# Kernel tuning notes

Measured on AMD Instinct MI355X. Metric: run time of the kernel, lower is better.

The kernel has to match this reference:

```python
import jax, jax.numpy as jnp
import numpy as np

NQ = 4
PI_HALF = np.pi / 2
HAD = jnp.array([[1, 1], [1, -1]], dtype=jnp.complex64) / np.sqrt(2)
CNOT = jnp.array([[1, 0, 0, 0], [0, 1, 0, 0], [0, 0, 0, 1], [0, 0, 1, 0]], dtype=jnp.complex64)
_bits = (np.arange(2 ** NQ)[:, None] >> np.arange(NQ - 1, -1, -1)[None, :]) & 1
ZSIGNS = jnp.asarray(1.0 - 2.0 * _bits, jnp.float32)  # [16, NQ]


def _ry(theta):
    c = jnp.cos(theta / 2).astype(jnp.complex64)
    s = jnp.sin(theta / 2).astype(jnp.complex64)
    return jnp.stack([jnp.stack([c, -s], -1), jnp.stack([s, c], -1)], -2)  # [...,2,2]


def _rot(phi, theta, omega):
    # PennyLane Rot = RZ(omega) @ RY(theta) @ RZ(phi)
    c = jnp.cos(theta / 2).astype(jnp.complex64)
    s = jnp.sin(theta / 2).astype(jnp.complex64)
    ep = jnp.exp(0.5j * phi).astype(jnp.complex64)
    eo = jnp.exp(0.5j * omega).astype(jnp.complex64)
    return jnp.stack([jnp.stack([jnp.conj(ep) * jnp.conj(eo) * c, -ep * jnp.conj(eo) * s]),
                      jnp.stack([jnp.conj(ep) * eo * s, ep * eo * c])])


def _cry(theta):
    # controlled-RY, batched: [B] -> [B,4,4], basis order (control, target)
    B = theta.shape[0]
    U = jnp.zeros((B, 4, 4), jnp.complex64).at[:, 0, 0].set(1.0).at[:, 1, 1].set(1.0)
    return U.at[:, 2:, 2:].set(_ry(theta))


def _apply1(state, U, wire):
    s = jnp.moveaxis(state, wire + 1, 1)
    shp = s.shape
    s = s.reshape(shp[0], 2, -1)
    s = jnp.einsum('ij,bjk->bik', U, s) if U.ndim == 2 else jnp.einsum('bij,bjk->bik', U, s)
    return jnp.moveaxis(s.reshape(shp), 1, wire + 1)


def _apply2(state, U, q0, q1):
    s = jnp.moveaxis(state, (q0 + 1, q1 + 1), (1, 2))
    shp = s.shape
    s = s.reshape(shp[0], 4, -1)
    s = jnp.einsum('ij,bjk->bik', U, s) if U.ndim == 2 else jnp.einsum('bij,bjk->bik', U, s)
    return jnp.moveaxis(s.reshape(shp), (1, 2), (q0 + 1, q1 + 1))


def _init_state(B):
    s = jnp.zeros((B, 2 ** NQ), jnp.complex64).at[:, 0].set(1.0)
    return s.reshape((B,) + (2,) * NQ)


def _zexp(state):
    p = state.reshape(state.shape[0], -1)
    p = p.real ** 2 + p.imag ** 2
    return p @ ZSIGNS  # [B, NQ]


def _attention_circuit(q, k, params):
    # q, k: [E, NQ] angles; params: [NQ, 3] shared
    s = _init_state(q.shape[0])
    for i in range(NQ):
        s = _apply1(s, _ry(q[:, i]), i)
    for i in range(NQ):
        s = _apply1(s, HAD, i)
    for i in range(NQ):
        s = _apply2(s, _cry(k[:, i]), i, (i + 1) % NQ)
    for i in range(NQ):
        s = _apply1(s, _rot(params[i, 0], params[i, 1], params[i, 2]), i)
    return _zexp(s)


def _entangle_circuit(x, params):
    # x: [N, NQ] angles; params: [n_layers, NQ, 3]
    s = _init_state(x.shape[0])
    for i in range(NQ):
        s = _apply1(s, _ry(x[:, i]), i)
    for l in range(params.shape[0]):
        for i in range(NQ - 1):
            s = _apply2(s, CNOT, i, i + 1)
        for i in range(NQ):
            s = _apply1(s, _rot(params[l, i, 0], params[l, i, 1], params[l, i, 2]), i)
        s = _apply2(s, CNOT, 0, NQ - 1)  # n_qubits >= 4
    return _zexp(s)


def _path_circuit(x, params):
    # x: [N, NQ]; params: [3, NQ, 3]
    s = _init_state(x.shape[0])
    for i in range(NQ):
        s = _apply1(s, HAD, i)
    for i in range(NQ):
        s = _apply1(s, _ry(x[:, i]), i)
    for l in range(3):
        for i in range(NQ):
            s = _apply1(s, _rot(params[l, i, 0], params[l, i, 1], params[l, i, 2]), i)
        for i in range(NQ - 1):
            s = _apply2(s, CNOT, i, i + 1)
    return _zexp(s)


def _forward(x, W_in, b_in, lin_W, lin_b, qproj_W, qproj_b, ent_params,
             attq_W, attq_b, attk_W, attk_b, att_qp, path_params,
             path_in_W, path_in_b, path_out_W, path_out_b, out_W, out_b, edge_index):
    N = x.shape[0]
    loops = jnp.arange(N, dtype=edge_index.dtype)
    ei = jnp.concatenate([edge_index, jnp.stack([loops, loops])], axis=1)  # add_self_loops
    src, dst = ei[0], ei[1]
    h = jax.nn.relu(x @ W_in.T + b_in)
    for l in range(lin_W.shape[0]):
        x_cls = h @ lin_W[l].T + lin_b[l]
        xq = _entangle_circuit(jnp.tanh(h[:, :NQ]) * PI_HALF, ent_params[l])
        x_comb = x_cls + xq @ qproj_W[l].T + qproj_b[l]
        q = jnp.tanh(h @ attq_W[l].T + attq_b[l]) * PI_HALF
        k = jnp.tanh(h @ attk_W[l].T + attk_b[l]) * PI_HALF
        scores = _attention_circuit(q[src], k[dst], att_qp[l]).mean(axis=1)  # [E]
        att = jax.nn.softmax(scores)  # global softmax over all edges (faithful)
        h = jax.ops.segment_sum(att[:, None] * x_comb[src], dst, num_segments=N)
        h = jax.nn.relu(h)  # dropout is identity at eval
    pq = jnp.tanh(h @ path_in_W.T + path_in_b) * PI_HALF
    h = _path_circuit(pq, path_params) @ path_out_W.T + path_out_b
    return h @ out_W.T + out_b


def setup_inputs() -> dict:
    key = jax.random.key(0)
    ks = jax.random.split(key, 22)
    N, E, D_in, D_h, D_out, L = 20000, 300000, 64, 128, 32, 2
    w = lambda k, shape: jax.random.normal(k, shape, jnp.float32) * 0.1
    return {
        'x': jax.random.normal(ks[0], (N, D_in), jnp.float32),
        'W_in': w(ks[1], (D_h, D_in)), 'b_in': w(ks[2], (D_h,)),
        'lin_W': w(ks[3], (L, D_h, D_h)), 'lin_b': w(ks[4], (L, D_h)),
        'qproj_W': w(ks[5], (L, D_h, NQ)), 'qproj_b': w(ks[6], (L, D_h)),
        'ent_params': w(ks[7], (L, 2, NQ, 3)),
        'attq_W': w(ks[8], (L, NQ, D_h)), 'attq_b': w(ks[9], (L, NQ)),
        'attk_W': w(ks[10], (L, NQ, D_h)), 'attk_b': w(ks[11], (L, NQ)),
        'att_qp': w(ks[12], (L, NQ, 3)),
        'path_params': w(ks[13], (3, NQ, 3)),
        'path_in_W': w(ks[14], (NQ, D_h)), 'path_in_b': w(ks[15], (NQ,)),
        'path_out_W': w(ks[16], (D_h, NQ)), 'path_out_b': w(ks[17], (D_h,)),
        'out_W': w(ks[18], (D_out, D_h)), 'out_b': w(ks[19], (D_out,)),
        'edge_index': jax.random.randint(ks[20], (2, E), 0, N, dtype=jnp.int32),
    }


def reference(x, W_in, b_in, lin_W, lin_b, qproj_W, qproj_b, ent_params,
              attq_W, attq_b, attk_W, attk_b, att_qp, path_params,
              path_in_W, path_in_b, path_out_W, path_out_b, out_W, out_b, edge_index):
    return _forward(x, W_in, b_in, lin_W, lin_b, qproj_W, qproj_b, ent_params,
                    attq_W, attq_b, attk_W, attk_b, att_qp, path_params,
                    path_in_W, path_in_b, path_out_W, path_out_b, out_W, out_b, edge_index)
```

## Files before the change

### kernel.cpp

```cpp
#include <hip/hip_runtime.h>
#include <math.h>

#define PI_HALF 1.57079632679489662f

__device__ __forceinline__ float fast_tanh(float x) {
    float e = __expf(2.f * x);
    return 1.f - 2.f * __builtin_amdgcn_rcpf(e + 1.f);
}


__device__ __forceinline__ void prod_init(float sr[16],
        float c0, float s0, float c1, float s1,
        float c2, float s2, float c3, float s3) {
    float p2[4];
    p2[0] = c0 * c1; p2[1] = c0 * s1; p2[2] = s0 * c1; p2[3] = s0 * s1;
    float p3[8];
#pragma unroll
    for (int j = 0; j < 4; ++j) { p3[2 * j] = p2[j] * c2; p3[2 * j + 1] = p2[j] * s2; }
#pragma unroll
    for (int j = 0; j < 8; ++j) { sr[2 * j] = p3[j] * c3; sr[2 * j + 1] = p3[j] * s3; }
}

template<int M>
__device__ __forceinline__ void had_r(float sr[16]) {
    const float r = 0.70710678118654752f;
#pragma unroll
    for (int i = 0; i < 16; ++i) {
        if (i & M) continue;
        const int j = i | M;
        float ar = sr[i], br = sr[j];
        sr[i] = (ar + br) * r;
        sr[j] = (ar - br) * r;
    }
}

template<int MC, int MT>
__device__ __forceinline__ void cry_r(float sr[16], float c, float s) {
#pragma unroll
    for (int i = 0; i < 16; ++i) {
        if (!(i & MC) || (i & MT)) continue;
        const int j = i | MT;
        float ar = sr[i], br = sr[j];
        sr[i] = c * ar - s * br;
        sr[j] = s * ar + c * br;
    }
}

template<int MC, int MT>
__device__ __forceinline__ void cnot_r(float sr[16]) {
#pragma unroll
    for (int i = 0; i < 16; ++i) {
        if (!(i & MC) || (i & MT)) continue;
        const int j = i | MT;
        float t = sr[i]; sr[i] = sr[j]; sr[j] = t;
    }
}

template<int MC, int MT>
__device__ __forceinline__ void cnot_g(float sr[16], float si[16]) {
#pragma unroll
    for (int i = 0; i < 16; ++i) {
        if (!(i & MC) || (i & MT)) continue;
        const int j = i | MT;
        float tr = sr[i], ti = si[i];
        sr[i] = sr[j]; si[i] = si[j];
        sr[j] = tr;    si[j] = ti;
    }
}

template<int M>
__device__ __forceinline__ void rot_pre(float sr[16], float si[16], const float* __restrict__ u) {
    const float u00r = u[0], u00i = u[1], u01r = u[2], u01i = u[3];
    const float u10r = u[4], u10i = u[5], u11r = u[6], u11i = u[7];
#pragma unroll
    for (int i = 0; i < 16; ++i) {
        if (i & M) continue;
        const int j = i | M;
        float ar = sr[i], ai = si[i], br = sr[j], bi = si[j];
        sr[i] = u00r * ar - u00i * ai + u01r * br - u01i * bi;
        si[i] = u00r * ai + u00i * ar + u01r * bi + u01i * br;
        sr[j] = u10r * ar - u10i * ai + u11r * br - u11i * bi;
        si[j] = u10r * ai + u10i * ar + u11r * bi + u11i * br;
    }
}

template<int M>
__device__ __forceinline__ void rot_first(float sr[16], float si[16], const float* __restrict__ u) {
    const float u00r = u[0], u00i = u[1], u01r = u[2], u01i = u[3];
    const float u10r = u[4], u10i = u[5], u11r = u[6], u11i = u[7];
#pragma unroll
    for (int i = 0; i < 16; ++i) {
        if (i & M) continue;
        const int j = i | M;
        float ar = sr[i], br = sr[j];
        sr[i] = u00r * ar + u01r * br;
        si[i] = u00i * ar + u01i * br;
        sr[j] = u10r * ar + u11r * br;
        si[j] = u10i * ar + u11i * br;
    }
}

__device__ __forceinline__ void zexp_g(const float sr[16], const float si[16], float z[4]) {
    float p[16];
#pragma unroll
    for (int i = 0; i < 16; ++i) p[i] = sr[i] * sr[i] + si[i] * si[i];
    z[0] = z[1] = z[2] = z[3] = 0.f;
#pragma unroll
    for (int i = 0; i < 16; ++i) {
        z[0] += (i & 8) ? -p[i] : p[i];
        z[1] += (i & 4) ? -p[i] : p[i];
        z[2] += (i & 2) ? -p[i] : p[i];
        z[3] += (i & 1) ? -p[i] : p[i];
    }
}


__global__ void k_fsi(const int* __restrict__ ei, int* __restrict__ cur,
                      int* __restrict__ srcs, int* __restrict__ inv, int E, int EP,
                      const float* __restrict__ entp, const float* __restrict__ attqp,
                      const float* __restrict__ pparm,
                      const float* __restrict__ outW, const float* __restrict__ outb,
                      const float* __restrict__ poW, const float* __restrict__ pob,
                      float* __restrict__ rotbuf, float* __restrict__ M,
                      float* __restrict__ v,
                      const float* __restrict__ x, const float* __restrict__ W,
                      const float* __restrict__ b, float* __restrict__ h,
                      int N, int eblocks) {
    __shared__ float xs[32 * 64];
    const int bb = blockIdx.x;
    const int tid = threadIdx.x;
    if (bb < eblocks) {
        int e = bb * 256 + tid;
        if (e < EP) {
            int s_, d_;
            if (e < E) { s_ = ei[e]; d_ = ei[E + e]; } else { s_ = d_ = e - E; }
            int pos = atomicAdd(&cur[d_], 1);
            srcs[pos] = s_;
            inv[e] = pos;
        }
        return;
    }
    if (bb == eblocks) {
        const int t = tid;
        if (t < 36) {
            const float* p;
            if (t < 16)      p = entp  + t * 3;
            else if (t < 24) p = attqp + (t - 16) * 3;
            else             p = pparm + (t - 24) * 3;
            float phi = p[0], theta = p[1], omega = p[2];
            float st, ct; sincosf(0.5f * theta, &st, &ct);
            float sp, cp; sincosf(0.5f * (phi + omega), &sp, &cp);
            float sm, cm; sincosf(0.5f * (phi - omega), &sm, &cm);
            float* u = rotbuf + t * 8;
            u[0] =  ct * cp;  u[1] = -ct * sp;
            u[2] = -st * cm;  u[3] = -st * sm;
            u[4] =  st * cm;  u[5] = -st * sm;
            u[6] =  ct * cp;  u[7] =  ct * sp;
        } else if (t >= 64 && t < 192) {
            int t2 = t - 64;
            int o = t2 >> 2, i = t2 & 3;
            float acc = 0.f;
            for (int j = 0; j < 128; ++j) acc += outW[o * 128 + j] * poW[j * 4 + i];
            M[t2] = acc;
        } else if (t >= 192 && t < 224) {
            int o = t - 192;
            float acc = outb[o];
            for (int j = 0; j < 128; ++j) acc += outW[o * 128 + j] * pob[j];
            v[o] = acc;
        }
        return;
    }
    const int base = (bb - eblocks - 1) * 32;
    for (int idx = tid; idx < 32 * 64; idx += 256) {
        int n = base + (idx >> 6);
        xs[idx] = (n < N) ? x[(size_t)n * 64 + (idx & 63)] : 0.f;
    }
    __syncthreads();
    const int ch = tid & 127;
    const int half = tid >> 7;
    float acc[16];
#pragma unroll
    for (int n = 0; n < 16; ++n) acc[n] = 0.f;
    const float4* wr4 = (const float4*)(W + ch * 64);
    for (int c4 = 0; c4 < 16; ++c4) {
        float4 w = wr4[c4];
#pragma unroll
        for (int n = 0; n < 16; ++n) {
            float4 hv = *(const float4*)&xs[(half * 16 + n) * 64 + c4 * 4];
            acc[n] += w.x * hv.x + w.y * hv.y + w.z * hv.z + w.w * hv.w;
        }
    }
    const float bbv = b[ch];
#pragma unroll
    for (int n = 0; n < 16; ++n) {
        int node = base + half * 16 + n;
        if (node < N) h[(size_t)node * 128 + ch] = fmaxf(acc[n] + bbv, 0.f);
    }
}

#define HS_STRIDE 132
__global__ void k_entlin(const float* __restrict__ h, const float* __restrict__ rotE2,
                         const float* __restrict__ linW, const float* __restrict__ linb,
                         const float* __restrict__ qpW, const float* __restrict__ qpb,
                         const float* __restrict__ aqW, const float* __restrict__ aqb,
                         const float* __restrict__ akW, const float* __restrict__ akb,
                         float* __restrict__ xcomb, float* __restrict__ qbuf,
                         float* __restrict__ kbuf, int N) {
    __shared__ float hs[16 * HS_STRIDE];
    __shared__ float xqs[16 * 4];
    const int base = blockIdx.x * 16;
    const int tid = threadIdx.x;
    for (int idx = tid; idx < 16 * 32; idx += 128) {
        int n = idx >> 5, c4 = idx & 31;
        int node = base + n;
        float4 hv = (node < N) ? *(const float4*)&h[(size_t)node * 128 + c4 * 4]
                               : make_float4(0.f, 0.f, 0.f, 0.f);
        *(float4*)&hs[n * HS_STRIDE + c4 * 4] = hv;
    }
    __syncthreads();
    if (tid < 64) {
#pragma unroll
        for (int rep = 0; rep < 2; ++rep) {
            const int dt = tid + rep * 64;
            const int nl = dt >> 3;
            const int which = dt & 7;
            const int qi = which & 3;
            const float4* Wp4 = (const float4*)(((which < 4) ? aqW : akW) + qi * 128);
            float dot = (which < 4) ? aqb[qi] : akb[qi];
            for (int c4 = 0; c4 < 32; ++c4) {
                float4 w = Wp4[c4];
                float4 hv = *(const float4*)&hs[nl * HS_STRIDE + c4 * 4];
                dot += w.x * hv.x + w.y * hv.y + w.z * hv.z + w.w * hv.w;
            }
            int node = base + nl;
            if (node < N) {
                float halfang = fast_tanh(dot) * (0.5f * PI_HALF);
                float s, c; __sincosf(halfang, &s, &c);
                float* dst = ((which < 4) ? qbuf : kbuf) + (size_t)node * 8 + qi * 2;
                dst[0] = c; dst[1] = s;
            }
        }
    } else if (tid < 80) {
        const int nl = tid - 64;
        if (base + nl < N) {
            float4 hv = *(const float4*)&hs[nl * HS_STRIDE];
            float c0, s0, c1, s1, c2, s2, c3, s3;
            { float a = fast_tanh(hv.x) * (0.5f * PI_HALF); __sincosf(a, &s0, &c0); }
            { float a = fast_tanh(hv.y) * (0.5f * PI_HALF); __sincosf(a, &s1, &c1); }
            { float a = fast_tanh(hv.z) * (0.5f * PI_HALF); __sincosf(a, &s2, &c2); }
            { float a = fast_tanh(hv.w) * (0.5f * PI_HALF); __sincosf(a, &s3, &c3); }
            float sr[16], si[16];
            prod_init(sr, c0, s0, c1, s1, c2, s2, c3, s3);
            cnot_r<8, 4>(sr); cnot_r<4, 2>(sr); cnot_r<2, 1>(sr);
            rot_first<8>(sr, si, rotE2);
            rot_pre<4>(sr, si, rotE2 + 8);
            rot_pre<2>(sr, si, rotE2 + 16);
            rot_pre<1>(sr, si, rotE2 + 24);
            cnot_g<8, 1>(sr, si);
            cnot_g<8, 4>(sr, si); cnot_g<4, 2>(sr, si); cnot_g<2, 1>(sr, si);
            const float* P = rotE2 + 32;
            rot_pre<8>(sr, si, P);
            rot_pre<4>(sr, si, P + 8);
            rot_pre<2>(sr, si, P + 16);
            rot_pre<1>(sr, si, P + 24);
            cnot_g<8, 1>(sr, si);
            float z[4]; zexp_g(sr, si, z);
            xqs[nl * 4 + 0] = z[0]; xqs[nl * 4 + 1] = z[1];
            xqs[nl * 4 + 2] = z[2]; xqs[nl * 4 + 3] = z[3];
        }
    }
    __syncthreads();
    const int lane = tid & 63;
    const int nh = tid >> 6;
    const int ch0 = lane, ch1 = lane + 64;
    float acc0[8], acc1[8];
#pragma unroll
    for (int n = 0; n < 8; ++n) { acc0[n] = 0.f; acc1[n] = 0.f; }
    const float4* w04 = (const float4*)(linW + ch0 * 128);
    const float4* w14 = (const float4*)(linW + ch1 * 128);
    for (int c4 = 0; c4 < 32; ++c4) {
        float4 wa = w04[c4];
        float4 wb = w14[c4];
#pragma unroll
        for (int n = 0; n < 8; ++n) {
            float4 hv = *(const float4*)&hs[(nh * 8 + n) * HS_STRIDE + c4 * 4];
            acc0[n] += wa.x * hv.x + wa.y * hv.y + wa.z * hv.z + wa.w * hv.w;
            acc1[n] += wb.x * hv.x + wb.y * hv.y + wb.z * hv.z + wb.w * hv.w;
        }
    }
    const float b0 = linb[ch0] + qpb[ch0];
    const float b1 = linb[ch1] + qpb[ch1];
    const float q00 = qpW[ch0 * 4 + 0], q01 = qpW[ch0 * 4 + 1];
    const float q02 = qpW[ch0 * 4 + 2], q03 = qpW[ch0 * 4 + 3];
    const float q10 = qpW[ch1 * 4 + 0], q11 = qpW[ch1 * 4 + 1];
    const float q12 = qpW[ch1 * 4 + 2], q13 = qpW[ch1 * 4 + 3];
#pragma unroll
    for (int n = 0; n < 8; ++n) {
        const int nl = nh * 8 + n;
        const int node = base + nl;
        if (node < N) {
            float x0 = xqs[nl * 4 + 0], x1 = xqs[nl * 4 + 1];
            float x2 = xqs[nl * 4 + 2], x3 = xqs[nl * 4 + 3];
            xcomb[(size_t)node * 128 + ch0] = acc0[n] + b0
                + q00 * x0 + q01 * x1 + q02 * x2 + q03 * x3;
            xcomb[(size_t)node * 128 + ch1] = acc1[n] + b1
                + q10 * x0 + q11 * x1 + q12 * x2 + q13 * x3;
        }
    }
}

__global__ void k_att(const float* __restrict__ qb, const float* __restrict__ kb,
                      const int* __restrict__ ei, const float* __restrict__ RA,
                      const int* __restrict__ inv, float* __restrict__ escore,
                      float* __restrict__ sumexp, int E, int EP) {
    __shared__ float red[4];
    int e = blockIdx.x * blockDim.x + threadIdx.x;
    float ex = 0.f;
    if (e < EP) {
        int s_, d_;
        if (e < E) { s_ = ei[e]; d_ = ei[E + e]; } else { s_ = d_ = e - E; }
        float4 qa = *(const float4*)&qb[(size_t)s_ * 8];
        float4 qc = *(const float4*)&qb[(size_t)s_ * 8 + 4];
        float4 ka = *(const float4*)&kb[(size_t)d_ * 8];
        float4 kc = *(const float4*)&kb[(size_t)d_ * 8 + 4];
        float sr[16], si[16];
        prod_init(sr, qa.x, qa.y, qa.z, qa.w, qc.x, qc.y, qc.z, qc.w);
        had_r<8>(sr); had_r<4>(sr); had_r<2>(sr); had_r<1>(sr);
        cry_r<8, 4>(sr, ka.x, ka.y);
        cry_r<4, 2>(sr, ka.z, ka.w);
        cry_r<2, 1>(sr, kc.x, kc.y);
        cry_r<1, 8>(sr, kc.z, kc.w);
        rot_first<8>(sr, si, RA);
        rot_pre<4>(sr, si, RA + 8);
        rot_pre<2>(sr, si, RA + 16);
        rot_pre<1>(sr, si, RA + 24);
        float p0  = sr[0]  * sr[0]  + si[0]  * si[0];
        float p1  = sr[1]  * sr[1]  + si[1]  * si[1];
        float p2  = sr[2]  * sr[2]  + si[2]  * si[2];
        float p4  = sr[4]  * sr[4]  + si[4]  * si[4];
        float p8  = sr[8]  * sr[8]  + si[8]  * si[8];
        float p7  = sr[7]  * sr[7]  + si[7]  * si[7];
        float p11 = sr[11] * sr[11] + si[11] * si[11];
        float p13 = sr[13] * sr[13] + si[13] * si[13];
        float p14 = sr[14] * sr[14] + si[14] * si[14];
        float p15 = sr[15] * sr[15] + si[15] * si[15];
        float sc = (p0 - p15) + 0.5f * ((p1 + p2 + p4 + p8) - (p7 + p11 + p13 + p14));
        ex = __expf(sc);
        escore[inv[e]] = ex;
    }
    float wsum = ex;
#pragma unroll
    for (int d = 32; d; d >>= 1) wsum += __shfl_xor(wsum, d, 64);
    if ((threadIdx.x & 63) == 0) red[threadIdx.x >> 6] = wsum;
    __syncthreads();
    if (threadIdx.x == 0) atomicAdd(sumexp, red[0] + red[1] + red[2] + red[3]);
}


__global__ void k_hist(const int* __restrict__ ei, int* __restrict__ cnt, int E, int EP) {
    int e = blockIdx.x * blockDim.x + threadIdx.x;
    if (e >= EP) return;
    int d_ = (e < E) ? ei[E + e] : e - E;
    atomicAdd(&cnt[d_], 1);
}

__global__ void k_scan(const int* __restrict__ cnt, int* __restrict__ off,
                       int* __restrict__ cur, int N) {
    __shared__ int tot[1024];
    const int t = threadIdx.x;
    const int chunk = (N + 1023) >> 10;
    const int s0 = t * chunk;
    const int s1 = min(s0 + chunk, N);
    int sum = 0;
    for (int i = s0; i < s1; ++i) sum += cnt[i];
    tot[t] = sum;
    __syncthreads();
    for (int d = 1; d < 1024; d <<= 1) {
        int v = (t >= d) ? tot[t - d] : 0;
        __syncthreads();
        tot[t] += v;
        __syncthreads();
    }
    int run = (t == 0) ? 0 : tot[t - 1];
    for (int i = s0; i < s1; ++i) {
        off[i] = run; cur[i] = run;
        run += cnt[i];
    }
}

__global__ void k_gather(const float* __restrict__ xcomb, const int* __restrict__ srcs,
                         const float* __restrict__ escore, const int* __restrict__ off,
                         const int* __restrict__ cnt, const float* __restrict__ sumexp,
                         float* __restrict__ h) {
    __shared__ int sS[128];
    __shared__ float wS[128];
    const int b = blockIdx.x;
    const int tid = threadIdx.x;
    const int start = off[b];
    const int num = cnt[b];
    float acc = 0.f;
    for (int base = 0; base < num; base += 128) {
        int m = min(128, num - base);
        if (tid < m) {
            sS[tid] = srcs[start + base + tid];
            wS[tid] = escore[start + base + tid];
        }
        __syncthreads();
        for (int i = 0; i < m; ++i)
            acc += wS[i] * xcomb[(size_t)sS[i] * 128 + tid];
        __syncthreads();
    }
    const float invS = __builtin_amdgcn_rcpf(sumexp[0]);
    h[(size_t)b * 128 + tid] = fmaxf(acc * invS, 0.f);
}

__global__ void k_tail(const float* __restrict__ h, const float* __restrict__ piW,
                       const float* __restrict__ pib, const float* __restrict__ RP,
                       const float* __restrict__ M, const float* __restrict__ v,
                       float* __restrict__ out, int N) {
    __shared__ float pqS[64 * 8];
    __shared__ float zS[64 * 4];
    __shared__ float MS[128];
    __shared__ float vS[32];
    const int tid = threadIdx.x;
    const int base = blockIdx.x * 64;
    if (tid < 128) MS[tid] = M[tid];
    else if (tid < 160) vS[tid - 128] = v[tid - 128];
    {
        const int nl = tid >> 2, i = tid & 3;
        const int node = base + nl;
        if (node < N) {
            float dot = pib[i];
            const float4* w4 = (const float4*)(piW + i * 128);
            const float4* h4 = (const float4*)(h + (size_t)node * 128);
#pragma unroll 8
            for (int c4 = 0; c4 < 32; ++c4) {
                float4 w = w4[c4];
                float4 hv = h4[c4];
                dot += w.x * hv.x + w.y * hv.y + w.z * hv.z + w.w * hv.w;
            }
            float halfang = fast_tanh(dot) * (0.5f * PI_HALF);
            float s, c; __sincosf(halfang, &s, &c);
            pqS[nl * 8 + i * 2]     = c;
            pqS[nl * 8 + i * 2 + 1] = s;
        }
    }
    __syncthreads();
    if (tid < 64 && base + tid < N) {
        const float r = 0.70710678118654752f;
        float c0 = pqS[tid * 8 + 0], s0 = pqS[tid * 8 + 1];
        float c1 = pqS[tid * 8 + 2], s1 = pqS[tid * 8 + 3];
        float c2 = pqS[tid * 8 + 4], s2 = pqS[tid * 8 + 5];
        float c3 = pqS[tid * 8 + 6], s3 = pqS[tid * 8 + 7];
        float u0 = r * (c0 - s0), w0 = r * (c0 + s0);
        float u1 = r * (c1 - s1), w1 = r * (c1 + s1);
        float u2 = r * (c2 - s2), w2 = r * (c2 + s2);
        float u3 = r * (c3 - s3), w3 = r * (c3 + s3);
        float sr[16], si[16];
        prod_init(sr, u0, w0, u1, w1, u2, w2, u3, w3);
        rot_first<8>(sr, si, RP);
        rot_pre<4>(sr, si, RP + 8);
        rot_pre<2>(sr, si, RP + 16);
        rot_pre<1>(sr, si, RP + 24);
        cnot_g<8, 4>(sr, si); cnot_g<4, 2>(sr, si); cnot_g<2, 1>(sr, si);
#pragma unroll
        for (int l = 1; l < 3; ++l) {
            const float* P = RP + l * 32;
            rot_pre<8>(sr, si, P);
            rot_pre<4>(sr, si, P + 8);
            rot_pre<2>(sr, si, P + 16);
            rot_pre<1>(sr, si, P + 24);
            cnot_g<8, 4>(sr, si); cnot_g<4, 2>(sr, si); cnot_g<2, 1>(sr, si);
        }
        float z[4]; zexp_g(sr, si, z);
        zS[tid * 4 + 0] = z[0]; zS[tid * 4 + 1] = z[1];
        zS[tid * 4 + 2] = z[2]; zS[tid * 4 + 3] = z[3];
    }
    __syncthreads();
#pragma unroll
    for (int k = 0; k < 8; ++k) {
        int flat = k * 256 + tid;
        int nl = flat >> 5;
        int o = flat & 31;
        int node = base + nl;
        if (node < N) {
            out[(size_t)node * 32 + o] = vS[o]
                + MS[o * 4 + 0] * zS[nl * 4 + 0] + MS[o * 4 + 1] * zS[nl * 4 + 1]
                + MS[o * 4 + 2] * zS[nl * 4 + 2] + MS[o * 4 + 3] * zS[nl * 4 + 3];
        }
    }
}


extern "C" void kernel_launch(void* const* d_in, const int* in_sizes, int n_in,
                              void* d_out, int out_size, void* d_ws, size_t ws_size,
                              hipStream_t stream) {
    const float* x     = (const float*)d_in[0];
    const float* W_in  = (const float*)d_in[1];
    const float* b_in  = (const float*)d_in[2];
    const float* linW  = (const float*)d_in[3];
    const float* linb  = (const float*)d_in[4];
    const float* qpW   = (const float*)d_in[5];
    const float* qpb   = (const float*)d_in[6];
    const float* entp  = (const float*)d_in[7];
    const float* aqW   = (const float*)d_in[8];
    const float* aqb   = (const float*)d_in[9];
    const float* akW   = (const float*)d_in[10];
    const float* akb   = (const float*)d_in[11];
    const float* attqp = (const float*)d_in[12];
    const float* pparm = (const float*)d_in[13];
    const float* piW   = (const float*)d_in[14];
    const float* pib   = (const float*)d_in[15];
    const float* poW   = (const float*)d_in[16];
    const float* pob   = (const float*)d_in[17];
    const float* outW  = (const float*)d_in[18];
    const float* outb  = (const float*)d_in[19];
    const int*   ei    = (const int*)d_in[20];

    const int N  = in_sizes[0] / 64;
    const int E  = in_sizes[20] / 2;
    const int EP = E + N;

    float* ws     = (float*)d_ws;
    float* h      = ws;
    float* xcomb  = h      + (size_t)N * 128;
    float* qbuf   = xcomb  + (size_t)N * 128;
    float* kbuf   = qbuf   + (size_t)N * 8;
    float* escore = kbuf   + (size_t)N * 8;
    float* rotbuf = escore + EP;
    float* Mm     = rotbuf + 36 * 8;
    float* vv     = Mm + 128;
    int*   cnt    = (int*)(vv + 32);
    float* sumexp = (float*)(cnt + N);
    int*   off    = (int*)(sumexp + 4);
    int*   cur    = off + N;
    int*   srcs   = cur + N;
    int*   inv    = srcs + EP;

    const float* rotE = rotbuf;
    const float* rotA = rotbuf + 128;
    const float* rotP = rotbuf + 192;

    const int nb16 = (N + 15) / 16;
    const int nb32 = (N + 31) / 32;
    const int ebl  = (EP + 255) / 256;

    hipMemsetAsync(cnt, 0, (size_t)(N + 4) * sizeof(int), stream);
    k_hist<<<ebl, 256, 0, stream>>>(ei, cnt, E, EP);
    k_scan<<<1, 1024, 0, stream>>>(cnt, off, cur, N);
    k_fsi<<<ebl + 1 + nb32, 256, 0, stream>>>(ei, cur, srcs, inv, E, EP,
                                              entp, attqp, pparm, outW, outb, poW, pob,
                                              rotbuf, Mm, vv, x, W_in, b_in, h, N, ebl);

    for (int l = 0; l < 2; ++l) {
        k_entlin<<<nb16, 128, 0, stream>>>(h, rotE + l * 64,
            linW + (size_t)l * 128 * 128, linb + l * 128,
            qpW + (size_t)l * 128 * 4, qpb + l * 128,
            aqW + (size_t)l * 4 * 128, aqb + l * 4,
            akW + (size_t)l * 4 * 128, akb + l * 4,
            xcomb, qbuf, kbuf, N);
        k_att<<<ebl, 256, 0, stream>>>(qbuf, kbuf, ei, rotA + l * 32, inv,
                                       escore, sumexp + l, E, EP);
        k_gather<<<N, 128, 0, stream>>>(xcomb, srcs, escore, off, cnt, sumexp + l, h);
    }

    k_tail<<<(N + 63) / 64, 256, 0, stream>>>(h, piW, pib, rotP, Mm, vv, (float*)d_out, N);
}
```

Before: 355.5 us.

## Fuse attention scoring into gather and defer softmax normalization to consumers

Per-edge attention score computation moves into the per-destination gather kernel, so the escore/inv buffers and the separate k_att launch disappear. Because the global sum is no longer known when h is written, normalization by 1/sumexp is deferred: h is stored unnormalized, and the next layer's entlin load or the tail projection rescales it. The memset is folded into k_fsi, and the CSR fill moves into layer 0's entlin launch as extra blocks. The score computation now runs per destination in a CSR-ordered block, which risks load imbalance on high-degree nodes and idle threads on low-degree ones.

```diff
diff --git a/kernel.cpp b/kernel.cpp
--- a/kernel.cpp
+++ b/kernel.cpp
@@ -115,9 +115,7 @@
 }
 
 
-__global__ void k_fsi(const int* __restrict__ ei, int* __restrict__ cur,
-                      int* __restrict__ srcs, int* __restrict__ inv, int E, int EP,
-                      const float* __restrict__ entp, const float* __restrict__ attqp,
+__global__ void k_fsi(const float* __restrict__ entp, const float* __restrict__ attqp,
                       const float* __restrict__ pparm,
                       const float* __restrict__ outW, const float* __restrict__ outb,
                       const float* __restrict__ poW, const float* __restrict__ pob,
@@ -125,22 +123,17 @@
                       float* __restrict__ v,
                       const float* __restrict__ x, const float* __restrict__ W,
                       const float* __restrict__ b, float* __restrict__ h,
-                      int N, int eblocks) {
+                      int* __restrict__ cnt, float* __restrict__ sumexp, int N) {
     __shared__ float xs[32 * 64];
     const int bb = blockIdx.x;
     const int tid = threadIdx.x;
-    if (bb < eblocks) {
-        int e = bb * 256 + tid;
-        if (e < EP) {
-            int s_, d_;
-            if (e < E) { s_ = ei[e]; d_ = ei[E + e]; } else { s_ = d_ = e - E; }
-            int pos = atomicAdd(&cur[d_], 1);
-            srcs[pos] = s_;
-            inv[e] = pos;
-        }
-        return;
-    }
-    if (bb == eblocks) {
+    {
+        const int gid = bb * 256 + tid;
+        const int T = gridDim.x * 256;
+        for (int i = gid; i < N; i += T) cnt[i] = 0;
+        if (gid < 4) sumexp[gid] = 0.f;
+    }
+    if (bb == 0) {
         const int t = tid;
         if (t < 36) {
             const float* p;
@@ -170,7 +163,7 @@
         }
         return;
     }
-    const int base = (bb - eblocks - 1) * 32;
+    const int base = (bb - 1) * 32;
     for (int idx = tid; idx < 32 * 64; idx += 256) {
         int n = base + (idx >> 6);
         xs[idx] = (n < N) ? x[(size_t)n * 64 + (idx & 63)] : 0.f;
@@ -195,6 +188,37 @@
     for (int n = 0; n < 16; ++n) {
         int node = base + half * 16 + n;
         if (node < N) h[(size_t)node * 128 + ch] = fmaxf(acc[n] + bbv, 0.f);
+    }
+}
+
+__global__ void k_hist(const int* __restrict__ ei, int* __restrict__ cnt, int E, int EP) {
+    int e = blockIdx.x * blockDim.x + threadIdx.x;
+    if (e >= EP) return;
+    int d_ = (e < E) ? ei[E + e] : e - E;
+    atomicAdd(&cnt[d_], 1);
+}
+
+__global__ void k_scan(const int* __restrict__ cnt, int* __restrict__ off,
+                       int* __restrict__ cur, int N) {
+    __shared__ int tot[1024];
+    const int t = threadIdx.x;
+    const int chunk = (N + 1023) >> 10;
+    const int s0 = t * chunk;
+    const int s1 = min(s0 + chunk, N);
+    int sum = 0;
+    for (int i = s0; i < s1; ++i) sum += cnt[i];
+    tot[t] = sum;
+    __syncthreads();
+    for (int d = 1; d < 1024; d <<= 1) {
+        int v = (t >= d) ? tot[t - d] : 0;
+        __syncthreads();
+        tot[t] += v;
+        __syncthreads();
+    }
+    int run = (t == 0) ? 0 : tot[t - 1];
+    for (int i = s0; i < s1; ++i) {
+        off[i] = run; cur[i] = run;
+        run += cnt[i];
     }
 }
 
@@ -205,16 +229,31 @@
                          const float* __restrict__ aqW, const float* __restrict__ aqb,
                          const float* __restrict__ akW, const float* __restrict__ akb,
                          float* __restrict__ xcomb, float* __restrict__ qbuf,
-                         float* __restrict__ kbuf, int N) {
+                         float* __restrict__ kbuf, int N,
+                         const float* __restrict__ sprev,
+                         int eblf, const int* __restrict__ ei,
+                         int* __restrict__ cur, int* __restrict__ srcs, int E, int EP) {
     __shared__ float hs[16 * HS_STRIDE];
     __shared__ float xqs[16 * 4];
-    const int base = blockIdx.x * 16;
     const int tid = threadIdx.x;
+    if (blockIdx.x < eblf) {
+        int e = blockIdx.x * 128 + tid;
+        if (e < EP) {
+            int s_, d_;
+            if (e < E) { s_ = ei[e]; d_ = ei[E + e]; } else { s_ = d_ = e - E; }
+            int pos = atomicAdd(&cur[d_], 1);
+            srcs[pos] = s_;
+        }
+        return;
+    }
+    const int base = (blockIdx.x - eblf) * 16;
+    const float scale = sprev ? __builtin_amdgcn_rcpf(sprev[0]) : 1.0f;
     for (int idx = tid; idx < 16 * 32; idx += 128) {
         int n = idx >> 5, c4 = idx & 31;
         int node = base + n;
         float4 hv = (node < N) ? *(const float4*)&h[(size_t)node * 128 + c4 * 4]
                                : make_float4(0.f, 0.f, 0.f, 0.f);
+        hv.x *= scale; hv.y *= scale; hv.z *= scale; hv.w *= scale;
         *(float4*)&hs[n * HS_STRIDE + c4 * 4] = hv;
     }
     __syncthreads();
@@ -309,114 +348,72 @@
     }
 }
 
-__global__ void k_att(const float* __restrict__ qb, const float* __restrict__ kb,
-                      const int* __restrict__ ei, const float* __restrict__ RA,
-                      const int* __restrict__ inv, float* __restrict__ escore,
-                      float* __restrict__ sumexp, int E, int EP) {
-    __shared__ float red[4];
-    int e = blockIdx.x * blockDim.x + threadIdx.x;
-    float ex = 0.f;
-    if (e < EP) {
-        int s_, d_;
-        if (e < E) { s_ = ei[e]; d_ = ei[E + e]; } else { s_ = d_ = e - E; }
-        float4 qa = *(const float4*)&qb[(size_t)s_ * 8];
-        float4 qc = *(const float4*)&qb[(size_t)s_ * 8 + 4];
-        float4 ka = *(const float4*)&kb[(size_t)d_ * 8];
-        float4 kc = *(const float4*)&kb[(size_t)d_ * 8 + 4];
-        float sr[16], si[16];
-        prod_init(sr, qa.x, qa.y, qa.z, qa.w, qc.x, qc.y, qc.z, qc.w);
-        had_r<8>(sr); had_r<4>(sr); had_r<2>(sr); had_r<1>(sr);
-        cry_r<8, 4>(sr, ka.x, ka.y);
-        cry_r<4, 2>(sr, ka.z, ka.w);
-        cry_r<2, 1>(sr, kc.x, kc.y);
-        cry_r<1, 8>(sr, kc.z, kc.w);
-        rot_first<8>(sr, si, RA);
-        rot_pre<4>(sr, si, RA + 8);
-        rot_pre<2>(sr, si, RA + 16);
-        rot_pre<1>(sr, si, RA + 24);
-        float p0  = sr[0]  * sr[0]  + si[0]  * si[0];
-        float p1  = sr[1]  * sr[1]  + si[1]  * si[1];
-        float p2  = sr[2]  * sr[2]  + si[2]  * si[2];
-        float p4  = sr[4]  * sr[4]  + si[4]  * si[4];
-        float p8  = sr[8]  * sr[8]  + si[8]  * si[8];
-        float p7  = sr[7]  * sr[7]  + si[7]  * si[7];
-        float p11 = sr[11] * sr[11] + si[11] * si[11];
-        float p13 = sr[13] * sr[13] + si[13] * si[13];
-        float p14 = sr[14] * sr[14] + si[14] * si[14];
-        float p15 = sr[15] * sr[15] + si[15] * si[15];
-        float sc = (p0 - p15) + 0.5f * ((p1 + p2 + p4 + p8) - (p7 + p11 + p13 + p14));
-        ex = __expf(sc);
-        escore[inv[e]] = ex;
-    }
-    float wsum = ex;
-#pragma unroll
-    for (int d = 32; d; d >>= 1) wsum += __shfl_xor(wsum, d, 64);
-    if ((threadIdx.x & 63) == 0) red[threadIdx.x >> 6] = wsum;
-    __syncthreads();
-    if (threadIdx.x == 0) atomicAdd(sumexp, red[0] + red[1] + red[2] + red[3]);
-}
-
-
-__global__ void k_hist(const int* __restrict__ ei, int* __restrict__ cnt, int E, int EP) {
-    int e = blockIdx.x * blockDim.x + threadIdx.x;
-    if (e >= EP) return;
-    int d_ = (e < E) ? ei[E + e] : e - E;
-    atomicAdd(&cnt[d_], 1);
-}
-
-__global__ void k_scan(const int* __restrict__ cnt, int* __restrict__ off,
-                       int* __restrict__ cur, int N) {
-    __shared__ int tot[1024];
-    const int t = threadIdx.x;
-    const int chunk = (N + 1023) >> 10;
-    const int s0 = t * chunk;
-    const int s1 = min(s0 + chunk, N);
-    int sum = 0;
-    for (int i = s0; i < s1; ++i) sum += cnt[i];
-    tot[t] = sum;
-    __syncthreads();
-    for (int d = 1; d < 1024; d <<= 1) {
-        int v = (t >= d) ? tot[t - d] : 0;
-        __syncthreads();
-        tot[t] += v;
-        __syncthreads();
-    }
-    int run = (t == 0) ? 0 : tot[t - 1];
-    for (int i = s0; i < s1; ++i) {
-        off[i] = run; cur[i] = run;
-        run += cnt[i];
-    }
-}
-
-__global__ void k_gather(const float* __restrict__ xcomb, const int* __restrict__ srcs,
-                         const float* __restrict__ escore, const int* __restrict__ off,
-                         const int* __restrict__ cnt, const float* __restrict__ sumexp,
-                         float* __restrict__ h) {
+__global__ void k_attg(const float* __restrict__ qb, const float* __restrict__ kb,
+                       const float* __restrict__ RA, const int* __restrict__ srcs,
+                       const int* __restrict__ off, const int* __restrict__ cnt,
+                       const float* __restrict__ xcomb, float* __restrict__ sumexp,
+                       float* __restrict__ h, int N) {
+    __shared__ float wS[128];
     __shared__ int sS[128];
-    __shared__ float wS[128];
+    __shared__ float red2[2];
     const int b = blockIdx.x;
     const int tid = threadIdx.x;
     const int start = off[b];
     const int num = cnt[b];
+    const float4 ka = *(const float4*)&kb[(size_t)b * 8];
+    const float4 kc = *(const float4*)&kb[(size_t)b * 8 + 4];
     float acc = 0.f;
+    float exsum = 0.f;
     for (int base = 0; base < num; base += 128) {
         int m = min(128, num - base);
         if (tid < m) {
-            sS[tid] = srcs[start + base + tid];
-            wS[tid] = escore[start + base + tid];
+            int s_ = srcs[start + base + tid];
+            sS[tid] = s_;
+            float4 qa = *(const float4*)&qb[(size_t)s_ * 8];
+            float4 qc = *(const float4*)&qb[(size_t)s_ * 8 + 4];
+            float sr[16], si[16];
+            prod_init(sr, qa.x, qa.y, qa.z, qa.w, qc.x, qc.y, qc.z, qc.w);
+            had_r<8>(sr); had_r<4>(sr); had_r<2>(sr); had_r<1>(sr);
+            cry_r<8, 4>(sr, ka.x, ka.y);
+            cry_r<4, 2>(sr, ka.z, ka.w);
+            cry_r<2, 1>(sr, kc.x, kc.y);
+            cry_r<1, 8>(sr, kc.z, kc.w);
+            rot_first<8>(sr, si, RA);
+            rot_pre<4>(sr, si, RA + 8);
+            rot_pre<2>(sr, si, RA + 16);
+            rot_pre<1>(sr, si, RA + 24);
+            float p0  = sr[0]  * sr[0]  + si[0]  * si[0];
+            float p1  = sr[1]  * sr[1]  + si[1]  * si[1];
+            float p2  = sr[2]  * sr[2]  + si[2]  * si[2];
+            float p4  = sr[4]  * sr[4]  + si[4]  * si[4];
+            float p8  = sr[8]  * sr[8]  + si[8]  * si[8];
+            float p7  = sr[7]  * sr[7]  + si[7]  * si[7];
+            float p11 = sr[11] * sr[11] + si[11] * si[11];
+            float p13 = sr[13] * sr[13] + si[13] * si[13];
+            float p14 = sr[14] * sr[14] + si[14] * si[14];
+            float p15 = sr[15] * sr[15] + si[15] * si[15];
+            float sc = (p0 - p15) + 0.5f * ((p1 + p2 + p4 + p8) - (p7 + p11 + p13 + p14));
+            float ex = __expf(sc);
+            wS[tid] = ex;
+            exsum += ex;
         }
         __syncthreads();
         for (int i = 0; i < m; ++i)
             acc += wS[i] * xcomb[(size_t)sS[i] * 128 + tid];
         __syncthreads();
     }
-    const float invS = __builtin_amdgcn_rcpf(sumexp[0]);
-    h[(size_t)b * 128 + tid] = fmaxf(acc * invS, 0.f);
+    h[(size_t)b * 128 + tid] = fmaxf(acc, 0.f);
+#pragma unroll
+    for (int d = 32; d; d >>= 1) exsum += __shfl_xor(exsum, d, 64);
+    if ((tid & 63) == 0) red2[tid >> 6] = exsum;
+    __syncthreads();
+    if (tid == 0) atomicAdd(sumexp, red2[0] + red2[1]);
 }
 
 __global__ void k_tail(const float* __restrict__ h, const float* __restrict__ piW,
                        const float* __restrict__ pib, const float* __restrict__ RP,
                        const float* __restrict__ M, const float* __restrict__ v,
+                       const float* __restrict__ sprev,
                        float* __restrict__ out, int N) {
     __shared__ float pqS[64 * 8];
     __shared__ float zS[64 * 4];
@@ -426,19 +423,21 @@
     const int base = blockIdx.x * 64;
     if (tid < 128) MS[tid] = M[tid];
     else if (tid < 160) vS[tid - 128] = v[tid - 128];
+    const float invS = __builtin_amdgcn_rcpf(sprev[0]);
     {
         const int nl = tid >> 2, i = tid & 3;
         const int node = base + nl;
         if (node < N) {
-            float dot = pib[i];
+            float raw = 0.f;
             const float4* w4 = (const float4*)(piW + i * 128);
             const float4* h4 = (const float4*)(h + (size_t)node * 128);
 #pragma unroll 8
             for (int c4 = 0; c4 < 32; ++c4) {
                 float4 w = w4[c4];
                 float4 hv = h4[c4];
-                dot += w.x * hv.x + w.y * hv.y + w.z * hv.z + w.w * hv.w;
+                raw += w.x * hv.x + w.y * hv.y + w.z * hv.z + w.w * hv.w;
             }
+            float dot = pib[i] + invS * raw;
             float halfang = fast_tanh(dot) * (0.5f * PI_HALF);
             float s, c; __sincosf(halfang, &s, &c);
             pqS[nl * 8 + i * 2]     = c;
@@ -526,8 +525,7 @@
     float* xcomb  = h      + (size_t)N * 128;
     float* qbuf   = xcomb  + (size_t)N * 128;
     float* kbuf   = qbuf   + (size_t)N * 8;
-    float* escore = kbuf   + (size_t)N * 8;
-    float* rotbuf = escore + EP;
+    float* rotbuf = kbuf   + (size_t)N * 8;
     float* Mm     = rotbuf + 36 * 8;
     float* vv     = Mm + 128;
     int*   cnt    = (int*)(vv + 32);
@@ -535,7 +533,6 @@
     int*   off    = (int*)(sumexp + 4);
     int*   cur    = off + N;
     int*   srcs   = cur + N;
-    int*   inv    = srcs + EP;
 
     const float* rotE = rotbuf;
     const float* rotA = rotbuf + 128;
@@ -544,25 +541,28 @@
     const int nb16 = (N + 15) / 16;
     const int nb32 = (N + 31) / 32;
     const int ebl  = (EP + 255) / 256;
-
-    hipMemsetAsync(cnt, 0, (size_t)(N + 4) * sizeof(int), stream);
+    const int eblf = (EP + 127) / 128;
+
+    k_fsi<<<nb32 + 1, 256, 0, stream>>>(entp, attqp, pparm, outW, outb, poW, pob,
+                                        rotbuf, Mm, vv, x, W_in, b_in, h,
+                                        cnt, sumexp, N);
     k_hist<<<ebl, 256, 0, stream>>>(ei, cnt, E, EP);
     k_scan<<<1, 1024, 0, stream>>>(cnt, off, cur, N);
-    k_fsi<<<ebl + 1 + nb32, 256, 0, stream>>>(ei, cur, srcs, inv, E, EP,
-                                              entp, attqp, pparm, outW, outb, poW, pob,
-                                              rotbuf, Mm, vv, x, W_in, b_in, h, N, ebl);
 
     for (int l = 0; l < 2; ++l) {
-        k_entlin<<<nb16, 128, 0, stream>>>(h, rotE + l * 64,
+        const int fillb = (l == 0) ? eblf : 0;
+        k_entlin<<<fillb + nb16, 128, 0, stream>>>(h, rotE + l * 64,
             linW + (size_t)l * 128 * 128, linb + l * 128,
             qpW + (size_t)l * 128 * 4, qpb + l * 128,
             aqW + (size_t)l * 4 * 128, aqb + l * 4,
             akW + (size_t)l * 4 * 128, akb + l * 4,
-            xcomb, qbuf, kbuf, N);
-        k_att<<<ebl, 256, 0, stream>>>(qbuf, kbuf, ei, rotA + l * 32, inv,
-                                       escore, sumexp + l, E, EP);
-        k_gather<<<N, 128, 0, stream>>>(xcomb, srcs, escore, off, cnt, sumexp + l, h);
-    }
-
-    k_tail<<<(N + 63) / 64, 256, 0, stream>>>(h, piW, pib, rotP, Mm, vv, (float*)d_out, N);
-}
+            xcomb, qbuf, kbuf, N,
+            (l == 0) ? (const float*)nullptr : (const float*)(sumexp + 0),
+            fillb, ei, cur, srcs, E, EP);
+        k_attg<<<N, 128, 0, stream>>>(qbuf, kbuf, rotA + l * 32, srcs, off, cnt,
+                                      xcomb, sumexp + l, h, N);
+    }
+
+    k_tail<<<(N + 63) / 64, 256, 0, stream>>>(h, piW, pib, rotP, Mm, vv,
+                                              sumexp + 1, (float*)d_out, N);
+}
```

After: 801.5 us. +125.5%, slower.
